# Performance work log

Measured on AMD Instinct MI355X. Metric: run time of the kernel, lower is better.

The kernel has to match this reference:

```python
import jax, jax.numpy as jnp
import numpy as np

N_CONCEPT = 15000  # graph has N_CONCEPT + 1 nodes
NNZ = 240016
EPS = 1e-12  # F.normalize eps


def setup_inputs() -> dict:
    key = jax.random.key(0)
    ks = jax.random.split(key, 10)
    B, S, E, O, D = 2048, 32, 1024, 1024, 1024
    s = 1.0 / np.sqrt(E)
    return {
        "data": jax.random.normal(ks[0], (B, S, E), jnp.float32),
        "seq_len": jax.random.randint(ks[1], (B,), 1, S + 1, jnp.int32),
        "conv_w": jax.random.normal(ks[2], (O, E), jnp.float32) * s,
        "conv_b": jax.random.normal(ks[3], (O,), jnp.float32) * s,
        "lin_w": jax.random.normal(ks[4], (D, O), jnp.float32) * s,
        "lin_b": jax.random.normal(ks[5], (D,), jnp.float32) * s,
        "gcn_bias": jnp.zeros((D,), jnp.float32),
        "H0": jax.random.normal(ks[6], (N_CONCEPT + 1, D), jnp.float32) * s,
        "indices": jax.random.randint(ks[7], (2, NNZ), 0, N_CONCEPT + 1, jnp.int32),
        "values": jax.random.uniform(ks[8], (NNZ,), jnp.float32),
    }


def reference(data, seq_len, conv_w, conv_b, lin_w, lin_b, gcn_bias, H0, indices, values):
    # --- CNN phrase encoder ---
    # conv1d kernel_size=1 == per-token linear: (B,S,E)x(O,E) -> (B,S,O)
    x = jax.nn.relu(jnp.einsum("bse,oe->bso", data, conv_w) + conv_b)
    x = jnp.max(x, axis=1)                              # max over sequence -> (B,O)
    x = jax.nn.relu(x @ lin_w.T + lin_b)                # (B,D)
    norm = jnp.linalg.norm(x, axis=1, keepdims=True)
    phrase = x / jnp.maximum(norm, EPS)                 # L2 normalize

    # --- sparse Laplacian GCN: L @ H0 + bias ---
    rows, cols = indices[0], indices[1]
    msgs = values[:, None] * H0[cols]                   # (nnz, D)
    graph = jax.ops.segment_sum(msgs, rows, num_segments=N_CONCEPT + 1) + gcn_bias

    # --- bilinear score: (B,D) @ (D, N+1) ---
    logits = phrase @ graph.T
    return logits
```

## Files before the change

### kernel.cpp

```cpp
#include <hip/hip_runtime.h>
#include <stdint.h>

typedef __attribute__((ext_vector_type(8))) __bf16 bf16x8;
typedef __attribute__((ext_vector_type(4))) float floatx4;

#define GLOBAL_AS __attribute__((address_space(1)))
#define LDS_AS __attribute__((address_space(3)))

#define CAP 96
#define N1 15001
#define NPAD 15104

__device__ __forceinline__ unsigned short f2bf(float x) {
  unsigned int u = __builtin_bit_cast(unsigned int, x);
  u += 0x7FFFu + ((u >> 16) & 1u);
  return (unsigned short)(u >> 16);
}
__device__ __forceinline__ unsigned int pk2(float lo, float hi) {
  return (unsigned)f2bf(lo) | ((unsigned)f2bf(hi) << 16);
}

__device__ __forceinline__ void stage_tile(const unsigned short* g, int ld, int row0, int k0,
                                           bf16x8* lds, int tid) {
  const int lane = tid & 63;
  const int w = tid >> 6;
#pragma unroll
  for (int j = 0; j < 2; ++j) {
    const int c = j * 256 + w * 64;
    const int kg = c >> 7;
    const int mbase = c & 127;
    const unsigned short* src = g + ((size_t)(row0 + mbase + lane) * ld + k0 + kg * 8);
    __builtin_amdgcn_global_load_lds((const GLOBAL_AS void*)src, (LDS_AS void*)(lds + c),
                                     16, 0, 0);
  }
}

template <int MODE>
__launch_bounds__(256, 2)
__global__ void gemm_bt(const void* __restrict__ Aptr,
                        const unsigned short* __restrict__ Bm,
                        const float* __restrict__ bias,
                        float* __restrict__ outF,
                        unsigned short* __restrict__ outU,
                        int nValid) {
  __shared__ bf16x8 As[2][512];
  __shared__ bf16x8 Bs[2][512];
  const int tid = threadIdx.x;
  const int lane = tid & 63;
  const int w = tid >> 6;
  const int wm = w >> 1, wn = w & 1;
  const int quad = lane >> 4, col = lane & 15;

  int bx = blockIdx.x, by = blockIdx.y;
  if ((gridDim.y & 7) == 0) {
    const unsigned L = (unsigned)by * gridDim.x + bx;
    const unsigned i = L >> 3, xk = L & 7;
    bx = i % gridDim.x;
    by = (i / gridDim.x) * 8 + xk;
  }
  const int m0 = by * 128, n0 = bx * 128;
  const int K = 1024;

  floatx4 acc[4][4];
#pragma unroll
  for (int a = 0; a < 4; ++a)
#pragma unroll
    for (int b = 0; b < 4; ++b) acc[a][b] = 0;

  auto stage = [&](int buf, int k0) {
    if (MODE == 0) {
      const int row = tid >> 1, kh = tid & 1;
      const float* src = (const float*)Aptr + (size_t)(m0 + row) * K + k0 + kh * 16;
      float4 v0 = ((const float4*)src)[0];
      float4 v1 = ((const float4*)src)[1];
      float4 v2 = ((const float4*)src)[2];
      float4 v3 = ((const float4*)src)[3];
      stage_tile(Bm, K, n0, k0, Bs[buf], tid);
      uint4 c0, c1;
      c0.x = pk2(v0.x, v0.y); c0.y = pk2(v0.z, v0.w);
      c0.z = pk2(v1.x, v1.y); c0.w = pk2(v1.z, v1.w);
      c1.x = pk2(v2.x, v2.y); c1.y = pk2(v2.z, v2.w);
      c1.z = pk2(v3.x, v3.y); c1.w = pk2(v3.z, v3.w);
      ((uint4*)As[buf])[(kh * 2) * 128 + row] = c0;
      ((uint4*)As[buf])[(kh * 2 + 1) * 128 + row] = c1;
    } else {
      stage_tile((const unsigned short*)Aptr, K, m0, k0, As[buf], tid);
      stage_tile(Bm, K, n0, k0, Bs[buf], tid);
    }
  };

  stage(0, 0);
  int cur = 0;
  for (int k0 = 0; k0 < K; k0 += 32) {
    __syncthreads();
    if (k0 + 32 < K) stage(cur ^ 1, k0 + 32);
    bf16x8 af[4], bfr[4];
#pragma unroll
    for (int t = 0; t < 4; ++t) af[t] = As[cur][quad * 128 + wm * 64 + t * 16 + col];
#pragma unroll
    for (int t = 0; t < 4; ++t) bfr[t] = Bs[cur][quad * 128 + wn * 64 + t * 16 + col];
#pragma unroll
    for (int mt = 0; mt < 4; ++mt)
#pragma unroll
      for (int nt = 0; nt < 4; ++nt)
        acc[mt][nt] = __builtin_amdgcn_mfma_f32_16x16x32_bf16(af[mt], bfr[nt], acc[mt][nt], 0, 0, 0);
    cur ^= 1;
  }

  if (MODE == 0 || MODE == 3) {
    float bv[4];
#pragma unroll
    for (int nt = 0; nt < 4; ++nt) bv[nt] = bias[n0 + wn * 64 + nt * 16 + col];
#pragma unroll
    for (int g = 0; g < 2; ++g) {
#pragma unroll
      for (int nt = 0; nt < 4; ++nt) {
        float v = -3.4e38f;
#pragma unroll
        for (int mh = 0; mh < 2; ++mh) {
          const int mt = 2 * g + mh;
#pragma unroll
          for (int r = 0; r < 4; ++r) v = fmaxf(v, acc[mt][nt][r]);
        }
        v += bv[nt];
        v = fmaxf(v, __shfl_xor(v, 16, 64));
        v = fmaxf(v, __shfl_xor(v, 32, 64));
        v = fmaxf(v, 0.0f);
        if (quad == 0) {
          const int b = (m0 >> 5) + wm * 2 + g;
          outU[b * 1024 + n0 + wn * 64 + nt * 16 + col] = f2bf(v);
        }
      }
    }
  } else if (MODE == 1) {
    float bv[4];
#pragma unroll
    for (int nt = 0; nt < 4; ++nt) bv[nt] = bias[n0 + wn * 64 + nt * 16 + col];
#pragma unroll
    for (int mt = 0; mt < 4; ++mt)
#pragma unroll
      for (int r = 0; r < 4; ++r) {
        const int row = m0 + wm * 64 + mt * 16 + quad * 4 + r;
#pragma unroll
        for (int nt = 0; nt < 4; ++nt)
          outF[(size_t)row * 1024 + n0 + wn * 64 + nt * 16 + col] =
              fmaxf(acc[mt][nt][r] + bv[nt], 0.0f);
      }
  } else {
#pragma unroll
    for (int mt = 0; mt < 4; ++mt)
#pragma unroll
      for (int r = 0; r < 4; ++r) {
        const size_t row = m0 + wm * 64 + mt * 16 + quad * 4 + r;
#pragma unroll
        for (int nt = 0; nt < 4; ++nt) {
          const int cg = n0 + wn * 64 + nt * 16 + col;
          if (cg < nValid) outF[row * (size_t)nValid + cg] = acc[mt][nt][r];
        }
      }
  }
}

__global__ void f32_to_bf16(const float* __restrict__ in, unsigned short* __restrict__ out, int n4) {
  const int i = blockIdx.x * 256 + threadIdx.x;
  if (i >= n4) return;
  const float4 v = ((const float4*)in)[i];
  uint2 p;
  p.x = pk2(v.x, v.y);
  p.y = pk2(v.z, v.w);
  ((uint2*)out)[i] = p;
}

__global__ void bucket_fill(const int* __restrict__ rows, int nnz,
                            int* __restrict__ cnt, int* __restrict__ bucket) {
  const int e = blockIdx.x * 256 + threadIdx.x;
  if (e >= nnz) return;
  const int r = rows[e];
  if ((unsigned)r >= (unsigned)N1) return;
  const int pos = atomicAdd(&cnt[r], 1);
  if (pos < CAP) bucket[r * CAP + pos] = e;
}

__global__ void build_graph(const int* __restrict__ cols,
                            const float* __restrict__ values,
                            const float* __restrict__ H0,
                            const float* __restrict__ gbias,
                            const int* __restrict__ cnt,
                            const int* __restrict__ bucket,
                            unsigned short* __restrict__ graph) {
  __shared__ int s_col[CAP];
  __shared__ float s_val[CAP];
  const int r = blockIdx.x;
  const int t = threadIdx.x;
  int n = (r < N1) ? cnt[r] : 0;
  if (n > CAP) n = CAP;
  if (t < n) {
    const int e = bucket[r * CAP + t];
    s_col[t] = cols[e];
    s_val[t] = values[e];
  }
  __syncthreads();
  float4 a = *(const float4*)(gbias + t * 4);
  for (int i = 0; i < n; ++i) {
    const int c = s_col[i];
    const float f = s_val[i];
    const float4 hv = *(const float4*)(H0 + (size_t)c * 1024 + t * 4);
    a.x += f * hv.x;
    a.y += f * hv.y;
    a.z += f * hv.z;
    a.w += f * hv.w;
  }
  uint2 p;
  p.x = pk2(a.x, a.y);
  p.y = pk2(a.z, a.w);
  *(uint2*)(graph + (size_t)r * 1024 + t * 4) = p;
}

__global__ void normalize_rows(const float* __restrict__ x, unsigned short* __restrict__ phrase) {
  const int b = blockIdx.x;
  const int t = threadIdx.x;
  const float4 v = *(const float4*)(x + (size_t)b * 1024 + t * 4);
  float ss = v.x * v.x + v.y * v.y + v.z * v.z + v.w * v.w;
#pragma unroll
  for (int o = 32; o > 0; o >>= 1) ss += __shfl_down(ss, o, 64);
  __shared__ float sred[4];
  if ((t & 63) == 0) sred[t >> 6] = ss;
  __syncthreads();
  const float tot = sred[0] + sred[1] + sred[2] + sred[3];
  const float inv = 1.0f / fmaxf(sqrtf(tot), 1e-12f);
  uint2 p;
  p.x = pk2(v.x * inv, v.y * inv);
  p.y = pk2(v.z * inv, v.w * inv);
  *(uint2*)(phrase + (size_t)b * 1024 + t * 4) = p;
}

extern "C" void kernel_launch(void* const* d_in, const int* in_sizes, int n_in,
                              void* d_out, int out_size, void* d_ws, size_t ws_size,
                              hipStream_t stream) {
  const float* data   = (const float*)d_in[0];
  const float* conv_w = (const float*)d_in[2];
  const float* conv_b = (const float*)d_in[3];
  const float* lin_w  = (const float*)d_in[4];
  const float* lin_b  = (const float*)d_in[5];
  const float* gbias  = (const float*)d_in[6];
  const float* H0     = (const float*)d_in[7];
  const int* indices  = (const int*)d_in[8];
  const float* values = (const float*)d_in[9];
  float* out = (float*)d_out;

  const int NNZ = in_sizes[9];

  char* ws = (char*)d_ws;
  char* ws0 = ws;
  unsigned short* conv_wb = (unsigned short*)ws; ws += (size_t)1024 * 1024 * 2;
  unsigned short* lin_wb  = (unsigned short*)ws; ws += (size_t)1024 * 1024 * 2;
  unsigned short* pooled  = (unsigned short*)ws; ws += (size_t)2048 * 1024 * 2;
  float* xbuf             = (float*)ws;          ws += (size_t)2048 * 1024 * 4;
  unsigned short* phrase  = (unsigned short*)ws; ws += (size_t)2048 * 1024 * 2;
  unsigned short* graph   = (unsigned short*)ws; ws += (size_t)NPAD * 1024 * 2;
  int* cnt                = (int*)ws;            ws += (size_t)NPAD * 4;
  int* bucket             = (int*)ws;            ws += (size_t)NPAD * CAP * 4;

  const size_t dataBfBytes = (size_t)2048 * 32 * 1024 * 2;
  unsigned short* data_bf = nullptr;
  if (ws_size >= (size_t)(ws - ws0) + dataBfBytes) {
    data_bf = (unsigned short*)ws;
    ws += dataBfBytes;
  }

  f32_to_bf16<<<1024, 256, 0, stream>>>(conv_w, conv_wb, 1024 * 1024 / 4);
  f32_to_bf16<<<1024, 256, 0, stream>>>(lin_w, lin_wb, 1024 * 1024 / 4);

  hipMemsetAsync(cnt, 0, (size_t)NPAD * 4, stream);
  bucket_fill<<<(NNZ + 255) / 256, 256, 0, stream>>>(indices, NNZ, cnt, bucket);
  build_graph<<<NPAD, 256, 0, stream>>>(indices + NNZ, values, H0, gbias, cnt, bucket, graph);

  if (data_bf) {
    f32_to_bf16<<<(2048 * 32 * 1024 / 4 + 255) / 256, 256, 0, stream>>>(
        data, data_bf, 2048 * 32 * 1024 / 4);
    gemm_bt<3><<<dim3(8, 512), 256, 0, stream>>>(data_bf, conv_wb, conv_b, nullptr, pooled, 1024);
  } else {
    gemm_bt<0><<<dim3(8, 512), 256, 0, stream>>>(data, conv_wb, conv_b, nullptr, pooled, 1024);
  }
  gemm_bt<1><<<dim3(8, 16), 256, 0, stream>>>(pooled, lin_wb, lin_b, xbuf, nullptr, 1024);
  normalize_rows<<<2048, 256, 0, stream>>>(xbuf, phrase);

  gemm_bt<2><<<dim3(118, 16), 256, 0, stream>>>(phrase, graph, nullptr, out, nullptr, N1);
}
```

Measured before the change: 1.022 ms.

## Triple-buffer LDS tiles with explicit vmcnt waits in bf16 GEMM modes

For the non-fp32 GEMM modes, the double-buffered K loop becomes a three-stage LDS ring. Two tiles are prefetched ahead using global_load_lds, and a partial s_waitcnt vmcnt(4) plus a raw s_barrier replaces the full __syncthreads drain. The goal is to keep more global loads in flight so load latency is hidden behind MFMA work. In exchange it uses 50% more LDS per block, which may reduce occupancy, and it depends on the hand-counted vmcnt value being correct.

```diff
diff --git a/kernel.cpp b/kernel.cpp
--- a/kernel.cpp
+++ b/kernel.cpp
@@ -43,8 +43,8 @@
                         float* __restrict__ outF,
                         unsigned short* __restrict__ outU,
                         int nValid) {
-  __shared__ bf16x8 As[2][512];
-  __shared__ bf16x8 Bs[2][512];
+  __shared__ bf16x8 As[3][512];
+  __shared__ bf16x8 Bs[3][512];
   const int tid = threadIdx.x;
   const int lane = tid & 63;
   const int w = tid >> 6;
@@ -67,8 +67,8 @@
 #pragma unroll
     for (int b = 0; b < 4; ++b) acc[a][b] = 0;
 
-  auto stage = [&](int buf, int k0) {
-    if (MODE == 0) {
+  if (MODE == 0) {
+    auto stage0 = [&](int buf, int k0) {
       const int row = tid >> 1, kh = tid & 1;
       const float* src = (const float*)Aptr + (size_t)(m0 + row) * K + k0 + kh * 16;
       float4 v0 = ((const float4*)src)[0];
@@ -83,28 +83,56 @@
       c1.z = pk2(v3.x, v3.y); c1.w = pk2(v3.z, v3.w);
       ((uint4*)As[buf])[(kh * 2) * 128 + row] = c0;
       ((uint4*)As[buf])[(kh * 2 + 1) * 128 + row] = c1;
-    } else {
-      stage_tile((const unsigned short*)Aptr, K, m0, k0, As[buf], tid);
-      stage_tile(Bm, K, n0, k0, Bs[buf], tid);
+    };
+    stage0(0, 0);
+    int cur = 0;
+    for (int k0 = 0; k0 < K; k0 += 32) {
+      __syncthreads();
+      if (k0 + 32 < K) stage0(cur ^ 1, k0 + 32);
+      bf16x8 af[4], bfr[4];
+#pragma unroll
+      for (int t = 0; t < 4; ++t) af[t] = As[cur][quad * 128 + wm * 64 + t * 16 + col];
+#pragma unroll
+      for (int t = 0; t < 4; ++t) bfr[t] = Bs[cur][quad * 128 + wn * 64 + t * 16 + col];
+#pragma unroll
+      for (int mt = 0; mt < 4; ++mt)
+#pragma unroll
+        for (int nt = 0; nt < 4; ++nt)
+          acc[mt][nt] = __builtin_amdgcn_mfma_f32_16x16x32_bf16(af[mt], bfr[nt], acc[mt][nt], 0, 0, 0);
+      cur ^= 1;
     }
-  };
-
-  stage(0, 0);
-  int cur = 0;
-  for (int k0 = 0; k0 < K; k0 += 32) {
-    __syncthreads();
-    if (k0 + 32 < K) stage(cur ^ 1, k0 + 32);
-    bf16x8 af[4], bfr[4];
-#pragma unroll
-    for (int t = 0; t < 4; ++t) af[t] = As[cur][quad * 128 + wm * 64 + t * 16 + col];
-#pragma unroll
-    for (int t = 0; t < 4; ++t) bfr[t] = Bs[cur][quad * 128 + wn * 64 + t * 16 + col];
-#pragma unroll
-    for (int mt = 0; mt < 4; ++mt)
-#pragma unroll
-      for (int nt = 0; nt < 4; ++nt)
-        acc[mt][nt] = __builtin_amdgcn_mfma_f32_16x16x32_bf16(af[mt], bfr[nt], acc[mt][nt], 0, 0, 0);
-    cur ^= 1;
+  } else {
+    const unsigned short* Am = (const unsigned short*)Aptr;
+    stage_tile(Am, K, m0, 0, As[0], tid);
+    stage_tile(Bm, K, n0, 0, Bs[0], tid);
+    stage_tile(Am, K, m0, 32, As[1], tid);
+    stage_tile(Bm, K, n0, 32, Bs[1], tid);
+    int cur = 0;
+    for (int k0 = 0; k0 < K; k0 += 32) {
+      if (k0 + 32 < K) {
+        asm volatile("s_waitcnt vmcnt(4)" ::: "memory");
+      } else {
+        asm volatile("s_waitcnt vmcnt(0)" ::: "memory");
+      }
+      __builtin_amdgcn_s_barrier();
+      __builtin_amdgcn_sched_barrier(0);
+      if (k0 + 64 < K) {
+        int nb = cur + 2; if (nb >= 3) nb -= 3;
+        stage_tile(Am, K, m0, k0 + 64, As[nb], tid);
+        stage_tile(Bm, K, n0, k0 + 64, Bs[nb], tid);
+      }
+      bf16x8 af[4], bfr[4];
+#pragma unroll
+      for (int t = 0; t < 4; ++t) af[t] = As[cur][quad * 128 + wm * 64 + t * 16 + col];
+#pragma unroll
+      for (int t = 0; t < 4; ++t) bfr[t] = Bs[cur][quad * 128 + wn * 64 + t * 16 + col];
+#pragma unroll
+      for (int mt = 0; mt < 4; ++mt)
+#pragma unroll
+        for (int nt = 0; nt < 4; ++nt)
+          acc[mt][nt] = __builtin_amdgcn_mfma_f32_16x16x32_bf16(af[mt], bfr[nt], acc[mt][nt], 0, 0, 0);
+      if (++cur == 3) cur = 0;
+    }
   }
 
   if (MODE == 0 || MODE == 3) {
```

New measurement: 1.028 ms. About the same (+0.5%).
